# Performance work log

Measured on AMD Instinct MI355X. Metric: run time of the kernel, lower is better.

## Reference

```python
import jax, jax.numpy as jnp
import numpy as np
from jax import lax

TAU = 2.0 * np.pi
S = 1024        # num_samples (anchor set)
B = 2048        # query batch
C = 8           # num_aug_channels
F = 10          # max_freq (also number of ODE output times)
D = 13 * 13 * C # 1352, augmented feature dim


def setup_inputs() -> dict:
    key = jax.random.key(0)
    k = jax.random.split(key, 5)
    data = jax.random.normal(k[0], (S, 1, 28, 28), jnp.float32)
    inputs = jax.random.normal(k[1], (B, 1, 28, 28), jnp.float32)
    conv_w = jax.random.normal(k[2], (C * F, 1, 3, 3), jnp.float32) * 0.1
    conv_b = jax.random.normal(k[3], (C * F,), jnp.float32) * 0.01
    # xavier_uniform_ on [S, D, F]: fan_in = D*F, fan_out = S*F
    bound = float(np.sqrt(6.0 / (D * F + S * F)))
    c_s = jax.random.uniform(k[4], (S, D, F), jnp.float32, -bound, bound)
    return {"data": data, "inputs": inputs, "conv_w": conv_w,
            "conv_b": conv_b, "c_s": c_s}


def _squash_in_sphere(v):
    norm = jnp.sqrt(jnp.sum(v * v, axis=1, keepdims=True) + 1e-6)
    return v * (jax.nn.sigmoid(norm) / norm)


def _adjusted_kernel(u, v):
    uu = jnp.sum(u * u, axis=1, keepdims=True)   # [m,1]
    vv = jnp.sum(v * v, axis=1, keepdims=True)   # [s,1]
    uv = u @ v.T                                  # [m,s]
    return jnp.exp(uv - uu / 2 - vv.T / 2) * uv


def _kernel(u, v):
    return _adjusted_kernel(_squash_in_sphere(u), _squash_in_sphere(v))


def reference(data, inputs, conv_w, conv_b, c_s):
    x = jnp.concatenate([data, inputs], axis=0)          # [N,1,28,28]
    out = lax.conv_general_dilated(
        x, conv_w, window_strides=(2, 2), padding='VALID',
        dimension_numbers=('NCHW', 'OIHW', 'NCHW')) + conv_b[None, :, None, None]
    N = out.shape[0]                                      # S + B
    # torch: reshape(N, F, -1) then transpose(1,2) -> psi_s [N, D, F]
    psi_s = jnp.transpose(out.reshape(N, F, -1), (0, 2, 1))
    coeffs = TAU * jnp.arange(F, dtype=psi_s.dtype)       # [F]

    def f(t, z):
        w = jnp.cos(t * coeffs)        # [F]
        c = c_s @ w                    # [S,D]
        psi = psi_s @ w                # [N,D]
        u = psi + z @ c                # [N,D]
        return _kernel(u, u[:S])       # [N,S]

    ts = jnp.linspace(0.0, 1.0, F).astype(psi_s.dtype)

    # Fixed-step RK4 between the output times (deterministic stand-in for the
    # adaptive odeint(rtol=1e-3, atol=1e-3) in the original).
    def rk4_step(z, th):
        t0, t1 = th
        h = t1 - t0
        k1 = f(t0, z)
        k2 = f(t0 + h / 2, z + (h / 2) * k1)
        k3 = f(t0 + h / 2, z + (h / 2) * k2)
        k4 = f(t1, z + h * k3)
        z_new = z + (h / 6) * (k1 + 2 * k2 + 2 * k3 + k4)
        return z_new, z_new

    z0 = jnp.zeros((N, S), psi_s.dtype)
    _, z_traj = lax.scan(rk4_step, z0, (ts[:-1], ts[1:]))
    zs = jnp.concatenate([z0[None], z_traj], axis=0)      # [F,N,S]

    # cost = square_norm(Augmenter) + sum_t flat_dot(z_t[:S] @ c_t, c_t) / F
    cost = jnp.sum(conv_w * conv_w) + jnp.sum(conv_b * conv_b)
    W_all = jnp.cos(ts[:, None] * coeffs[None, :])        # [F,F]
    c_all = jnp.einsum('ndf,tf->tnd', c_s, W_all)          # [F,S,D]
    cost = cost + jnp.einsum('tij,tjd,tid->', zs[:, :S], c_all, c_all) / F

    out_z = jnp.transpose(zs, (1, 0, 2)).reshape(N, F * S)[S:]  # [B, F*S]
    return out_z, cost
```

## Files before the change

kernel.cpp:

```cpp
#include <hip/hip_runtime.h>
#include <hip/hip_fp8.h>
#include <math.h>

#define S_ANCH 1024
#define B_QRY  2048
#define N_TOT  3072
#define D_DIM  1352
#define D_PAD  1408
#define F_NUM  10
#define N_TV   19
#define NPART  44
#define CSCALE 128.0f
#define CINV   (1.0f / 128.0f)

static const size_t SD    = (size_t)S_ANCH * D_DIM;
static const size_t NS    = (size_t)N_TOT * S_ANCH;
static const size_t CST   = (size_t)D_PAD * S_ANCH;
static const size_t PSIP  = (size_t)N_TOT * D_PAD;
static const size_t OUT_Z = (size_t)B_QRY * F_NUM * S_ANCH;

typedef __attribute__((ext_vector_type(8))) short bf16x8;
typedef __attribute__((ext_vector_type(4))) float f32x4;

struct W190 { float w[N_TV][F_NUM]; };

__device__ inline unsigned short f2bf(float x) {
    unsigned int u = __builtin_bit_cast(unsigned int, x);
    unsigned int r = (u + 0x7FFFu + ((u >> 16) & 1u)) >> 16;
    return (unsigned short)r;
}
__device__ inline float bf2f(unsigned short v) {
    unsigned int u = ((unsigned int)v) << 16;
    return __builtin_bit_cast(float, u);
}
__device__ inline unsigned char f2fp8(float x) {
    __hip_fp8_e4m3 q(x);
    return (unsigned char)q.__x;
}

__device__ __forceinline__ void stage16(const unsigned char* gp, unsigned char* lp) {
    __builtin_amdgcn_global_load_lds(
        (const __attribute__((address_space(1))) unsigned int*)(const void*)gp,
        (__attribute__((address_space(3))) unsigned int*)(void*)lp, 16, 0, 0);
}

__global__ __launch_bounds__(256) void init_kernel(float* __restrict__ z,
                                                   unsigned char* __restrict__ z8,
                                                   float* __restrict__ cost,
                                                   float* __restrict__ rowsqP,
                                                   unsigned short* __restrict__ psi0,
                                                   float* __restrict__ out) {
    size_t idx = (size_t)blockIdx.x * blockDim.x + threadIdx.x;
    size_t stride = (size_t)gridDim.x * blockDim.x;
    for (size_t i = idx; i < NS; i += stride) { z[i] = 0.f; z8[i] = 0; }
    const size_t NO = (size_t)B_QRY * S_ANCH;
    for (size_t i = idx; i < NO; i += stride) {
        size_t b = i >> 10, s = i & 1023;
        out[b * (size_t)(F_NUM * S_ANCH) + s] = 0.f;
    }
    const size_t NR = (size_t)NPART * N_TOT;
    for (size_t i = idx; i < NR; i += stride) rowsqP[i] = 0.f;
    const size_t NPAD = (size_t)N_TOT * (D_PAD - D_DIM);
    for (size_t i = idx; i < NPAD; i += stride) {
        size_t n = i / (D_PAD - D_DIM), c = i % (D_PAD - D_DIM);
        psi0[n * D_PAD + D_DIM + c] = 0;
    }
    if (idx == 0) cost[0] = 0.f;
}

__global__ __launch_bounds__(256) void c_all_kernel(const float* __restrict__ cs,
                                                    unsigned char* __restrict__ c8,
                                                    float* __restrict__ cfp, W190 W) {
    __shared__ float tile[32][65];
    int d0 = blockIdx.x * 64, s0 = blockIdx.y * 32;
    int t = threadIdx.x;
    int d_l = t & 63, s_base = t >> 6;
    int d = d0 + d_l;
    bool dok = (d < D_DIM);
    float creg[8][F_NUM];
#pragma unroll
    for (int it = 0; it < 8; it++) {
        int s = s0 + s_base + it * 4;
        const float* p = cs + ((size_t)s * D_DIM + d) * F_NUM;
#pragma unroll
        for (int f = 0; f < F_NUM; f++) creg[it][f] = dok ? p[f] : 0.f;
    }
    for (int j = 0; j < N_TV; j++) {
        float v[8];
#pragma unroll
        for (int it = 0; it < 8; it++) {
            float s = 0.f;
#pragma unroll
            for (int f = 0; f < F_NUM; f++) s += creg[it][f] * W.w[j][f];
            v[it] = s;
            tile[s_base + it * 4][d_l] = s;
        }
        if ((j & 1) == 0 && j >= 2 && dok) {
            int gi = (j >> 1) - 1;
#pragma unroll
            for (int it = 0; it < 8; it++)
                cfp[(size_t)gi * SD + (size_t)(s0 + s_base + it * 4) * D_DIM + d] = v[it];
        }
        __syncthreads();
        int s_l = t & 31, dr = t >> 5;
#pragma unroll
        for (int p8 = 0; p8 < 8; p8++) {
            int dd = dr + p8 * 8;
            c8[(size_t)j * CST + (size_t)(d0 + dd) * S_ANCH + s0 + s_l] =
                f2fp8(tile[s_l][dd] * CSCALE);
        }
        __syncthreads();
    }
}

__global__ __launch_bounds__(256) void conv_psi_all_kernel(const float* __restrict__ data,
                                                           const float* __restrict__ inputs,
                                                           const float* __restrict__ cw,
                                                           const float* __restrict__ cb,
                                                           unsigned short* __restrict__ psi_all,
                                                           W190 W) {
    __shared__ float wsh[720];
    __shared__ float bsh[80];
    for (int i = threadIdx.x; i < 720; i += 256) wsh[i] = cw[i];
    for (int i = threadIdx.x; i < 80; i += 256) bsh[i] = cb[i];
    __syncthreads();
    size_t idx = (size_t)blockIdx.x * 256 + threadIdx.x;
    if (idx >= (size_t)N_TOT * 8 * 169) return;
    int pos = (int)(idx % 169);
    int rest = (int)(idx / 169);
    int c8 = rest & 7;
    int n = rest >> 3;
    int oi = pos / 13, oj = pos % 13;
    const float* x = (n < S_ANCH) ? (data + (size_t)n * 784)
                                  : (inputs + (size_t)(n - S_ANCH) * 784);
    float vin[9];
#pragma unroll
    for (int kh = 0; kh < 3; kh++)
#pragma unroll
        for (int kw = 0; kw < 3; kw++)
            vin[kh * 3 + kw] = x[(2 * oi + kh) * 28 + (2 * oj + kw)];
    float s[F_NUM];
#pragma unroll
    for (int f = 0; f < F_NUM; f++) {
        int co = f * 8 + c8;
        float acc = bsh[co];
#pragma unroll
        for (int t = 0; t < 9; t++) acc += vin[t] * wsh[co * 9 + t];
        s[f] = acc;
    }
    size_t base = (size_t)n * D_PAD + c8 * 169 + pos;
#pragma unroll
    for (int j = 0; j < N_TV; j++) {
        float p = 0.f;
#pragma unroll
        for (int f = 0; f < F_NUM; f++) p += s[f] * W.w[j][f];
        psi_all[(size_t)j * PSIP + base] = f2bf(p);
    }
}

__global__ __launch_bounds__(256) void rowsq_psi_kernel(const unsigned short* __restrict__ psi0,
                                                        float* __restrict__ rowsqP,
                                                        unsigned char* __restrict__ u8) {
    int wv = threadIdx.x >> 6, lane = threadIdx.x & 63;
    int r = blockIdx.x * 4 + wv;
    const unsigned short* row = psi0 + (size_t)r * D_PAD;
    unsigned char* orow = u8 + (size_t)r * D_PAD;
    float s = 0.f;
    for (int c = lane; c < D_PAD / 8; c += 64) {
        int4 v = *(const int4*)(row + c * 8);
        const unsigned short* u = (const unsigned short*)&v;
        unsigned long long w = 0ull;
#pragma unroll
        for (int e = 0; e < 8; e++) {
            float f = bf2f(u[e]);
            s += f * f;
            w |= (unsigned long long)f2fp8(f) << (8 * e);
        }
        *(unsigned long long*)(orow + c * 8) = w;
    }
    s += __shfl_xor(s, 1); s += __shfl_xor(s, 2); s += __shfl_xor(s, 4);
    s += __shfl_xor(s, 8); s += __shfl_xor(s, 16); s += __shfl_xor(s, 32);
    if (lane == 0) rowsqP[r] = s;
}

struct GemmArgs {
    const unsigned char* A; const unsigned char* B;
    int lda, ldb, K;
    int gx;
    const unsigned short* psi16; unsigned char* u8; float* rowsqP;
    int do_cost;
    const float* cfp; float* cost;
    float* zcur; unsigned short* accb16; unsigned char* zt8; float* outp;
    int first, finish, tout; float alpha, h6;
};

template<int MODE>
__global__ __launch_bounds__(256) void mfma_gemm(GemmArgs g) {
    __shared__ __align__(16) unsigned char As[6][64][64];
    __shared__ __align__(16) unsigned char Bs[6][64][64];
    __shared__ float sclM[64], ahM[64], sclN[64], ahN[64];
    __shared__ float red4[4];
    const int nb = gridDim.x;
    const int lin = blockIdx.x;
    const int swz = (lin & 7) * (nb >> 3) + (lin >> 3);
    const int bx = swz % g.gx, by = swz / g.gx;
    const int bm = by * 64, bn = bx * 64;
    const int t = threadIdx.x;
    const int lane = t & 63, wv = t >> 6;
    const int wm = (wv >> 1) * 32, wn = (wv & 1) * 32;
    const int lr = lane & 15, lg = lane >> 4;
    const int srow = lane >> 2;
    const int gch = (lane & 3) ^ ((lane >> 3) & 3);

    if (MODE == 1) {
        if (t < 128) {
            int r = (t < 64) ? (bm + t) : (bn + (t - 64));
            float tot = 0.f;
#pragma unroll
            for (int c = 0; c < NPART; c++) tot += g.rowsqP[(size_t)c * N_TOT + r];
            float norm = sqrtf(tot + 1e-6f);
            float sg = 1.f / (1.f + __expf(-norm));
            float sc = sg / norm;
            float a = 0.5f * tot * sc * sc;
            if (t < 64) { sclM[t] = sc; ahM[t] = a; }
            else        { sclN[t - 64] = sc; ahN[t - 64] = a; }
        }
    }

    const bool docost = (MODE == 0) && g.do_cost && (bm < S_ANCH);
    unsigned short psi_r[2][4][2];
    float cfp_r[2][4][2];
    float zc_r[2][4][2];
    unsigned short ab_r[2][4][2];
    if (MODE == 0) {
#pragma unroll
        for (int i = 0; i < 2; i++)
#pragma unroll
            for (int reg = 0; reg < 4; reg++) {
                int m = bm + wm + i * 16 + lg * 4 + reg;
#pragma unroll
                for (int j = 0; j < 2; j++) {
                    int n = bn + wn + j * 16 + lr;
                    psi_r[i][reg][j] = g.psi16[(size_t)m * D_PAD + n];
                    if (docost)
                        cfp_r[i][reg][j] = (n < D_DIM) ? g.cfp[(size_t)m * D_DIM + n] : 0.f;
                }
            }
    } else if (MODE == 1) {
#pragma unroll
        for (int i = 0; i < 2; i++)
#pragma unroll
            for (int reg = 0; reg < 4; reg++) {
                int m = bm + wm + i * 16 + lg * 4 + reg;
#pragma unroll
                for (int j = 0; j < 2; j++) {
                    int n = bn + wn + j * 16 + lr;
                    size_t idx = (size_t)m * S_ANCH + n;
                    zc_r[i][reg][j] = g.zcur[idx];
                    ab_r[i][reg][j] = g.accb16[idx];
                }
            }
    }
    __builtin_amdgcn_sched_barrier(0);

    f32x4 acc[2][2];
#pragma unroll
    for (int i = 0; i < 2; i++)
#pragma unroll
        for (int j = 0; j < 2; j++) acc[i][j] = (f32x4){0.f, 0.f, 0.f, 0.f};

    const unsigned char* Abase = g.A + (size_t)(bm + wv * 16 + srow) * g.lda + gch * 16;
    const unsigned char* Bbase = g.B + (size_t)(bn + wv * 16 + srow) * g.ldb + gch * 16;

    auto STAGE = [&](int k) {
        int buf = k % 6;
        stage16(Abase + (k << 6), &As[buf][wv * 16][0]);
        stage16(Bbase + (k << 6), &Bs[buf][wv * 16][0]);
    };
    auto COMPUTE = [&](int k) {
        int buf = k % 6;
#pragma unroll
        for (int ks = 0; ks < 2; ks++) {
            int ch = ((ks << 1) + (lg >> 1)) ^ ((lr >> 1) & 3);
            int off = ch * 16 + (lg & 1) * 8;
            long a0 = *(const long*)&As[buf][wm + lr][off];
            long a1 = *(const long*)&As[buf][wm + 16 + lr][off];
            long b0 = *(const long*)&Bs[buf][wn + lr][off];
            long b1 = *(const long*)&Bs[buf][wn + 16 + lr][off];
            acc[0][0] = __builtin_amdgcn_mfma_f32_16x16x32_fp8_fp8(a0, b0, acc[0][0], 0, 0, 0);
            acc[0][1] = __builtin_amdgcn_mfma_f32_16x16x32_fp8_fp8(a0, b1, acc[0][1], 0, 0, 0);
            acc[1][0] = __builtin_amdgcn_mfma_f32_16x16x32_fp8_fp8(a1, b0, acc[1][0], 0, 0, 0);
            acc[1][1] = __builtin_amdgcn_mfma_f32_16x16x32_fp8_fp8(a1, b1, acc[1][1], 0, 0, 0);
        }
    };

    const int nt = g.K >> 6;
    STAGE(0); STAGE(1); STAGE(2); STAGE(3); STAGE(4);
    for (int k = 0; k < nt - 5; ++k) {
        asm volatile("s_waitcnt vmcnt(8)" ::: "memory");
        __builtin_amdgcn_s_barrier();
        __builtin_amdgcn_sched_barrier(0);
        STAGE(k + 5);
        COMPUTE(k);
    }
    asm volatile("s_waitcnt vmcnt(8)" ::: "memory");
    __builtin_amdgcn_s_barrier(); __builtin_amdgcn_sched_barrier(0);
    COMPUTE(nt - 5);
    asm volatile("s_waitcnt vmcnt(6)" ::: "memory");
    __builtin_amdgcn_s_barrier(); __builtin_amdgcn_sched_barrier(0);
    COMPUTE(nt - 4);
    asm volatile("s_waitcnt vmcnt(4)" ::: "memory");
    __builtin_amdgcn_s_barrier(); __builtin_amdgcn_sched_barrier(0);
    COMPUTE(nt - 3);
    asm volatile("s_waitcnt vmcnt(2)" ::: "memory");
    __builtin_amdgcn_s_barrier(); __builtin_amdgcn_sched_barrier(0);
    COMPUTE(nt - 2);
    asm volatile("s_waitcnt vmcnt(0)" ::: "memory");
    __builtin_amdgcn_s_barrier(); __builtin_amdgcn_sched_barrier(0);
    COMPUTE(nt - 1);

    if (MODE == 0) {
        float cst = 0.f;
#pragma unroll
        for (int i = 0; i < 2; i++) {
#pragma unroll
            for (int reg = 0; reg < 4; reg++) {
                int m = bm + wm + i * 16 + lg * 4 + reg;
                float sq = 0.f;
#pragma unroll
                for (int j = 0; j < 2; j++) {
                    int n = bn + wn + j * 16 + lr;
                    float v = acc[i][j][reg] * CINV;
                    bool nok = n < D_DIM;
                    if (docost) cst += v * cfp_r[i][reg][j];
                    if (nok) v += bf2f(psi_r[i][reg][j]);
                    else v = 0.f;
                    g.u8[(size_t)m * D_PAD + n] = f2fp8(v);
                    sq += v * v;
                }
                sq += __shfl_xor(sq, 1);
                sq += __shfl_xor(sq, 2);
                sq += __shfl_xor(sq, 4);
                sq += __shfl_xor(sq, 8);
                if (lr == 0)
                    g.rowsqP[(size_t)(bx * 2 + (wn >> 5)) * N_TOT + m] = sq;
            }
        }
        if (docost) {
            cst += __shfl_xor(cst, 1); cst += __shfl_xor(cst, 2);
            cst += __shfl_xor(cst, 4); cst += __shfl_xor(cst, 8);
            cst += __shfl_xor(cst, 16); cst += __shfl_xor(cst, 32);
            if (lane == 0) red4[wv] = cst;
            __syncthreads();
            if (t == 0) atomicAdd(g.cost, red4[0] + red4[1] + red4[2] + red4[3]);
        }
    } else if (MODE == 1) {
        __syncthreads();
#pragma unroll
        for (int i = 0; i < 2; i++) {
#pragma unroll
            for (int reg = 0; reg < 4; reg++) {
                int mi = wm + i * 16 + lg * 4 + reg;
                int m = bm + mi;
                float sm = sclM[mi], am = ahM[mi];
#pragma unroll
                for (int j = 0; j < 2; j++) {
                    int ni = wn + j * 16 + lr;
                    int n = bn + ni;
                    float uv = acc[i][j][reg] * sm * sclN[ni];
                    float kv = __expf(uv - am - ahN[ni]) * uv;
                    size_t idx = (size_t)m * S_ANCH + n;
                    if (!g.finish) {
                        float ab = g.first ? kv : (bf2f(ab_r[i][reg][j]) + 2.0f * kv);
                        g.accb16[idx] = f2bf(ab);
                        float zt = zc_r[i][reg][j] + g.alpha * kv;
                        g.zt8[idx] = f2fp8(zt);
                    } else {
                        float z = zc_r[i][reg][j] + g.h6 * (bf2f(ab_r[i][reg][j]) + kv);
                        g.zcur[idx] = z;
                        g.zt8[idx] = f2fp8(z);
                        if (m >= S_ANCH)
                            g.outp[(size_t)(m - S_ANCH) * (F_NUM * S_ANCH)
                                   + (size_t)g.tout * S_ANCH + n] = z;
                    }
                }
            }
        }
    } else {
        float s = 0.f;
#pragma unroll
        for (int i = 0; i < 2; i++)
#pragma unroll
            for (int reg = 0; reg < 4; reg++) {
                int m = bm + wm + i * 16 + lg * 4 + reg;
#pragma unroll
                for (int j = 0; j < 2; j++) {
                    int n = bn + wn + j * 16 + lr;
                    if (n < D_DIM)
                        s += acc[i][j][reg] * CINV * g.cfp[(size_t)m * D_DIM + n];
                }
            }
        s += __shfl_xor(s, 1); s += __shfl_xor(s, 2); s += __shfl_xor(s, 4);
        s += __shfl_xor(s, 8); s += __shfl_xor(s, 16); s += __shfl_xor(s, 32);
        if (lane == 0) red4[wv] = s;
        __syncthreads();
        if (t == 0) atomicAdd(g.cost, red4[0] + red4[1] + red4[2] + red4[3]);
    }
}

__global__ __launch_bounds__(256) void final_kernel(const float* __restrict__ cw,
                                                    const float* __restrict__ cb,
                                                    const float* __restrict__ cost,
                                                    float* __restrict__ out) {
    float s = 0.f;
    for (int i = threadIdx.x; i < 720; i += 256) s += cw[i] * cw[i];
    for (int i = threadIdx.x; i < 80; i += 256) s += cb[i] * cb[i];
    for (int o = 32; o > 0; o >>= 1) s += __shfl_down(s, o);
    __shared__ float red[4];
    if ((threadIdx.x & 63) == 0) red[threadIdx.x >> 6] = s;
    __syncthreads();
    if (threadIdx.x == 0) out[0] = red[0] + red[1] + red[2] + red[3] + cost[0] / 10.0f;
}

extern "C" void kernel_launch(void* const* d_in, const int* in_sizes, int n_in,
                              void* d_out, int out_size, void* d_ws, size_t ws_size,
                              hipStream_t stream) {
    (void)in_sizes; (void)n_in; (void)out_size; (void)ws_size;
    const float* data   = (const float*)d_in[0];
    const float* inputs = (const float*)d_in[1];
    const float* conv_w = (const float*)d_in[2];
    const float* conv_b = (const float*)d_in[3];
    const float* c_s    = (const float*)d_in[4];
    float* out = (float*)d_out;

    char* ws = (char*)d_ws;
    size_t off = 0;
    auto alloc = [&](size_t bytes) {
        char* p = ws + off; off += (bytes + 255) & ~(size_t)255; return p;
    };
    unsigned char*  c8_all  = (unsigned char*)alloc((size_t)N_TV * CST);
    float*          cfp_all = (float*)alloc((size_t)9 * SD * 4);
    unsigned short* psi_all = (unsigned short*)alloc((size_t)N_TV * PSIP * 2);
    unsigned char*  u8      = (unsigned char*)alloc(PSIP);
    float*          z_cur   = (float*)alloc(NS * 4);
    unsigned char*  z8      = (unsigned char*)alloc(NS);
    unsigned char*  zt8     = (unsigned char*)alloc(NS);
    unsigned short* accb16  = (unsigned short*)alloc(NS * 2);
    float*          rowsqP  = (float*)alloc((size_t)NPART * N_TOT * 4);
    float*          cost    = (float*)alloc(64);

    const double TAU_D = 6.2831853071795864769;
    float ts[F_NUM];
    for (int i = 0; i < F_NUM; i++) ts[i] = (float)((double)i / 9.0);
    W190 Wall;
    for (int j = 0; j < N_TV; j++) {
        float tt;
        if ((j & 1) == 0) tt = ts[j >> 1];
        else {
            int i = j >> 1;
            float h = ts[i + 1] - ts[i];
            tt = ts[i] + 0.5f * h;
        }
        for (int f = 0; f < F_NUM; f++) {
            float coeff = (float)(TAU_D * f);
            float targ = tt * coeff;
            Wall.w[j][f] = (float)cos((double)targ);
        }
    }

    init_kernel<<<2048, 256, 0, stream>>>(z_cur, z8, cost, rowsqP, psi_all, out);
    c_all_kernel<<<dim3(22, 32), 256, 0, stream>>>(c_s, c8_all, cfp_all, Wall);
    const int conv_blocks = (int)(((size_t)N_TOT * 8 * 169 + 255) / 256);
    conv_psi_all_kernel<<<conv_blocks, 256, 0, stream>>>(data, inputs, conv_w, conv_b,
                                                         psi_all, Wall);

    GemmArgs g0 = {};
    g0.lda = S_ANCH; g0.ldb = S_ANCH; g0.K = S_ANCH; g0.gx = 22;
    g0.u8 = u8; g0.rowsqP = rowsqP; g0.cost = cost;
    GemmArgs g1 = {};
    g1.A = u8; g1.B = u8; g1.lda = D_PAD; g1.ldb = D_PAD; g1.K = D_PAD; g1.gx = 16;
    g1.zcur = z_cur; g1.accb16 = accb16; g1.rowsqP = rowsqP;
    GemmArgs g2 = {};
    g2.A = z8; g2.B = c8_all + (size_t)18 * CST;
    g2.lda = S_ANCH; g2.ldb = S_ANCH; g2.K = S_ANCH; g2.gx = 22;
    g2.cfp = cfp_all + (size_t)8 * SD; g2.cost = cost;

    for (int i = 0; i < 9; i++) {
        float h = ts[i + 1] - ts[i];
        int js[4] = {2 * i, 2 * i + 1, 2 * i + 1, 2 * i + 2};
        float alphas[3] = {0.5f * h, 0.5f * h, h};
        for (int e = 0; e < 4; e++) {
            int j = js[e];
            const bool shortcut = (i == 0 && e == 0);
            if (shortcut) {
                rowsq_psi_kernel<<<N_TOT / 4, 256, 0, stream>>>(psi_all, rowsqP, u8);
            } else {
                g0.A = (e == 0) ? z8 : zt8;
                g0.B = c8_all + (size_t)j * CST;
                g0.psi16 = psi_all + (size_t)j * PSIP;
                g0.do_cost = (e == 0 && i >= 1) ? 1 : 0;
                g0.cfp = (i >= 1) ? (cfp_all + (size_t)(i - 1) * SD) : cfp_all;
                mfma_gemm<0><<<22 * 48, 256, 0, stream>>>(g0);
            }
            g1.first = (e == 0); g1.finish = (e == 3);
            g1.alpha = (e < 3) ? alphas[e] : 0.f;
            g1.h6 = h / 6.0f; g1.tout = i + 1;
            g1.zt8 = (e < 3) ? zt8 : z8;
            g1.outp = out;
            mfma_gemm<1><<<16 * 48, 256, 0, stream>>>(g1);
        }
    }
    mfma_gemm<2><<<22 * 16, 256, 0, stream>>>(g2);

    final_kernel<<<1, 256, 0, stream>>>(conv_w, conv_b, cost, out + OUT_Z);
}
```

Measured before the change: 1.675 ms.

## Store psi tables in fp8 and shrink GEMM LDS pipeline to four stages

Precomputed psi tables for all 19 evaluation times are now stored in fp8 instead of bf16, so they take half the memory and half the epilogue read traffic. The first step reads psi directly as the GEMM operand instead of copying it into a separate fp8 buffer. Separately, the MFMA GEMM's shared-memory ring drops from six to four stages, which lowers LDS use and may allow more resident blocks but hides less latency. The added fp8 rounding of psi lowers accuracy of the kernel inputs.

```diff
diff --git a/kernel.cpp b/kernel.cpp
--- a/kernel.cpp
+++ b/kernel.cpp
@@ -19,7 +19,6 @@
 static const size_t PSIP  = (size_t)N_TOT * D_PAD;
 static const size_t OUT_Z = (size_t)B_QRY * F_NUM * S_ANCH;
 
-typedef __attribute__((ext_vector_type(8))) short bf16x8;
 typedef __attribute__((ext_vector_type(4))) float f32x4;
 
 struct W190 { float w[N_TV][F_NUM]; };
@@ -37,6 +36,10 @@
     __hip_fp8_e4m3 q(x);
     return (unsigned char)q.__x;
 }
+__device__ inline float fp82f(unsigned char b) {
+    __hip_fp8_e4m3 q; q.__x = b;
+    return (float)q;
+}
 
 __device__ __forceinline__ void stage16(const unsigned char* gp, unsigned char* lp) {
     __builtin_amdgcn_global_load_lds(
@@ -48,7 +51,7 @@
                                                    unsigned char* __restrict__ z8,
                                                    float* __restrict__ cost,
                                                    float* __restrict__ rowsqP,
-                                                   unsigned short* __restrict__ psi0,
+                                                   unsigned char* __restrict__ psi0,
                                                    float* __restrict__ out) {
     size_t idx = (size_t)blockIdx.x * blockDim.x + threadIdx.x;
     size_t stride = (size_t)gridDim.x * blockDim.x;
@@ -117,7 +120,7 @@
                                                            const float* __restrict__ inputs,
                                                            const float* __restrict__ cw,
                                                            const float* __restrict__ cb,
-                                                           unsigned short* __restrict__ psi_all,
+                                                           unsigned char* __restrict__ psi_all,
                                                            W190 W) {
     __shared__ float wsh[720];
     __shared__ float bsh[80];
@@ -154,29 +157,23 @@
         float p = 0.f;
 #pragma unroll
         for (int f = 0; f < F_NUM; f++) p += s[f] * W.w[j][f];
-        psi_all[(size_t)j * PSIP + base] = f2bf(p);
-    }
-}
-
-__global__ __launch_bounds__(256) void rowsq_psi_kernel(const unsigned short* __restrict__ psi0,
-                                                        float* __restrict__ rowsqP,
-                                                        unsigned char* __restrict__ u8) {
+        psi_all[(size_t)j * PSIP + base] = f2fp8(p);
+    }
+}
+
+__global__ __launch_bounds__(256) void rowsq_psi_kernel(const unsigned char* __restrict__ psi0,
+                                                        float* __restrict__ rowsqP) {
     int wv = threadIdx.x >> 6, lane = threadIdx.x & 63;
     int r = blockIdx.x * 4 + wv;
-    const unsigned short* row = psi0 + (size_t)r * D_PAD;
-    unsigned char* orow = u8 + (size_t)r * D_PAD;
+    const unsigned char* row = psi0 + (size_t)r * D_PAD;
     float s = 0.f;
     for (int c = lane; c < D_PAD / 8; c += 64) {
-        int4 v = *(const int4*)(row + c * 8);
-        const unsigned short* u = (const unsigned short*)&v;
-        unsigned long long w = 0ull;
+        unsigned long long w = *(const unsigned long long*)(row + c * 8);
 #pragma unroll
         for (int e = 0; e < 8; e++) {
-            float f = bf2f(u[e]);
+            float f = fp82f((unsigned char)(w >> (8 * e)));
             s += f * f;
-            w |= (unsigned long long)f2fp8(f) << (8 * e);
-        }
-        *(unsigned long long*)(orow + c * 8) = w;
+        }
     }
     s += __shfl_xor(s, 1); s += __shfl_xor(s, 2); s += __shfl_xor(s, 4);
     s += __shfl_xor(s, 8); s += __shfl_xor(s, 16); s += __shfl_xor(s, 32);
@@ -187,7 +184,7 @@
     const unsigned char* A; const unsigned char* B;
     int lda, ldb, K;
     int gx;
-    const unsigned short* psi16; unsigned char* u8; float* rowsqP;
+    const unsigned char* psi8; unsigned char* u8; float* rowsqP;
     int do_cost;
     const float* cfp; float* cost;
     float* zcur; unsigned short* accb16; unsigned char* zt8; float* outp;
@@ -196,8 +193,8 @@
 
 template<int MODE>
 __global__ __launch_bounds__(256) void mfma_gemm(GemmArgs g) {
-    __shared__ __align__(16) unsigned char As[6][64][64];
-    __shared__ __align__(16) unsigned char Bs[6][64][64];
+    __shared__ __align__(16) unsigned char As[4][64][64];
+    __shared__ __align__(16) unsigned char Bs[4][64][64];
     __shared__ float sclM[64], ahM[64], sclN[64], ahN[64];
     __shared__ float red4[4];
     const int nb = gridDim.x;
@@ -228,7 +225,7 @@
     }
 
     const bool docost = (MODE == 0) && g.do_cost && (bm < S_ANCH);
-    unsigned short psi_r[2][4][2];
+    unsigned char psi_r[2][4][2];
     float cfp_r[2][4][2];
     float zc_r[2][4][2];
     unsigned short ab_r[2][4][2];
@@ -241,7 +238,7 @@
 #pragma unroll
                 for (int j = 0; j < 2; j++) {
                     int n = bn + wn + j * 16 + lr;
-                    psi_r[i][reg][j] = g.psi16[(size_t)m * D_PAD + n];
+                    psi_r[i][reg][j] = g.psi8[(size_t)m * D_PAD + n];
                     if (docost)
                         cfp_r[i][reg][j] = (n < D_DIM) ? g.cfp[(size_t)m * D_DIM + n] : 0.f;
                 }
@@ -273,12 +270,12 @@
     const unsigned char* Bbase = g.B + (size_t)(bn + wv * 16 + srow) * g.ldb + gch * 16;
 
     auto STAGE = [&](int k) {
-        int buf = k % 6;
+        int buf = k & 3;
         stage16(Abase + (k << 6), &As[buf][wv * 16][0]);
         stage16(Bbase + (k << 6), &Bs[buf][wv * 16][0]);
     };
     auto COMPUTE = [&](int k) {
-        int buf = k % 6;
+        int buf = k & 3;
 #pragma unroll
         for (int ks = 0; ks < 2; ks++) {
             int ch = ((ks << 1) + (lg >> 1)) ^ ((lr >> 1) & 3);
@@ -295,20 +292,14 @@
     };
 
     const int nt = g.K >> 6;
-    STAGE(0); STAGE(1); STAGE(2); STAGE(3); STAGE(4);
-    for (int k = 0; k < nt - 5; ++k) {
-        asm volatile("s_waitcnt vmcnt(8)" ::: "memory");
+    STAGE(0); STAGE(1); STAGE(2);
+    for (int k = 0; k < nt - 3; ++k) {
+        asm volatile("s_waitcnt vmcnt(4)" ::: "memory");
         __builtin_amdgcn_s_barrier();
         __builtin_amdgcn_sched_barrier(0);
-        STAGE(k + 5);
+        STAGE(k + 3);
         COMPUTE(k);
     }
-    asm volatile("s_waitcnt vmcnt(8)" ::: "memory");
-    __builtin_amdgcn_s_barrier(); __builtin_amdgcn_sched_barrier(0);
-    COMPUTE(nt - 5);
-    asm volatile("s_waitcnt vmcnt(6)" ::: "memory");
-    __builtin_amdgcn_s_barrier(); __builtin_amdgcn_sched_barrier(0);
-    COMPUTE(nt - 4);
     asm volatile("s_waitcnt vmcnt(4)" ::: "memory");
     __builtin_amdgcn_s_barrier(); __builtin_amdgcn_sched_barrier(0);
     COMPUTE(nt - 3);
@@ -333,7 +324,7 @@
                     float v = acc[i][j][reg] * CINV;
                     bool nok = n < D_DIM;
                     if (docost) cst += v * cfp_r[i][reg][j];
-                    if (nok) v += bf2f(psi_r[i][reg][j]);
+                    if (nok) v += fp82f(psi_r[i][reg][j]);
                     else v = 0.f;
                     g.u8[(size_t)m * D_PAD + n] = f2fp8(v);
                     sq += v * v;
@@ -440,7 +431,7 @@
     };
     unsigned char*  c8_all  = (unsigned char*)alloc((size_t)N_TV * CST);
     float*          cfp_all = (float*)alloc((size_t)9 * SD * 4);
-    unsigned short* psi_all = (unsigned short*)alloc((size_t)N_TV * PSIP * 2);
+    unsigned char*  psi_all = (unsigned char*)alloc((size_t)N_TV * PSIP);
     unsigned char*  u8      = (unsigned char*)alloc(PSIP);
     float*          z_cur   = (float*)alloc(NS * 4);
     unsigned char*  z8      = (unsigned char*)alloc(NS);
@@ -478,7 +469,7 @@
     g0.lda = S_ANCH; g0.ldb = S_ANCH; g0.K = S_ANCH; g0.gx = 22;
     g0.u8 = u8; g0.rowsqP = rowsqP; g0.cost = cost;
     GemmArgs g1 = {};
-    g1.A = u8; g1.B = u8; g1.lda = D_PAD; g1.ldb = D_PAD; g1.K = D_PAD; g1.gx = 16;
+    g1.lda = D_PAD; g1.ldb = D_PAD; g1.K = D_PAD; g1.gx = 16;
     g1.zcur = z_cur; g1.accb16 = accb16; g1.rowsqP = rowsqP;
     GemmArgs g2 = {};
     g2.A = z8; g2.B = c8_all + (size_t)18 * CST;
@@ -493,15 +484,17 @@
             int j = js[e];
             const bool shortcut = (i == 0 && e == 0);
             if (shortcut) {
-                rowsq_psi_kernel<<<N_TOT / 4, 256, 0, stream>>>(psi_all, rowsqP, u8);
+                rowsq_psi_kernel<<<N_TOT / 4, 256, 0, stream>>>(psi_all, rowsqP);
             } else {
                 g0.A = (e == 0) ? z8 : zt8;
                 g0.B = c8_all + (size_t)j * CST;
-                g0.psi16 = psi_all + (size_t)j * PSIP;
+                g0.psi8 = psi_all + (size_t)j * PSIP;
                 g0.do_cost = (e == 0 && i >= 1) ? 1 : 0;
                 g0.cfp = (i >= 1) ? (cfp_all + (size_t)(i - 1) * SD) : cfp_all;
                 mfma_gemm<0><<<22 * 48, 256, 0, stream>>>(g0);
             }
+            g1.A = shortcut ? psi_all : u8;
+            g1.B = shortcut ? psi_all : u8;
             g1.first = (e == 0); g1.finish = (e == 3);
             g1.alpha = (e < 3) ? alphas[e] : 0.f;
             g1.h6 = h / 6.0f; g1.tout = i + 1;
```

New measurement: 1.653 ms. Within noise of the previous version (-1.3%).
